# Performance work log

Measured on AMD Instinct MI355X. Metric: run time of the kernel, lower is better.

## Reference

```python
import jax, jax.numpy as jnp
import numpy as np

N, E, IN, H, ED = 50000, 800000, 128, 128, 3
EPS = 1e-5

def _gat_conv(x, src, dst, ea, W, a_src, a_dst, We, a_edge, bias):
    n = x.shape[0]
    # add self loops; self-loop edge_attr = per-feature mean (PyG fill_value='mean')
    loops = jnp.arange(n, dtype=src.dtype)
    s = jnp.concatenate([src, loops])
    d = jnp.concatenate([dst, loops])
    ea_full = jnp.concatenate([ea, jnp.broadcast_to(ea.mean(0), (n, ea.shape[1]))], 0)
    h = x @ W                       # [n, H]
    al_s = h @ a_src                # [n]
    al_d = h @ a_dst
    al_e = (ea_full @ We) @ a_edge  # [E+n]
    alpha = jax.nn.leaky_relu(al_s[s] + al_d[d] + al_e, 0.2)
    # segment softmax over destination nodes (every node has a self loop)
    amax = jax.ops.segment_max(alpha, d, num_segments=n)
    ex = jnp.exp(alpha - amax[d])
    denom = jax.ops.segment_sum(ex, d, num_segments=n)
    coef = ex / (denom[d] + 1e-16)
    out = jax.ops.segment_sum(h[s] * coef[:, None], d, num_segments=n)
    return out + bias

def _bn(x, gamma, beta):
    mu = x.mean(0)
    var = ((x - mu) ** 2).mean(0)
    return (x - mu) * jax.lax.rsqrt(var + EPS) * gamma + beta

def setup_inputs():
    key = jax.random.key(0)
    ks = jax.random.split(key, 40)
    inp = {
        "x": jax.random.normal(ks[0], (N, IN), jnp.float32),
        "edge_index": jax.random.randint(ks[1], (2, E), 0, N, dtype=jnp.int32),
        "batch": jnp.zeros((N,), jnp.int32),
        "edge_attr": jax.random.normal(ks[2], (E, ED), jnp.float32),
    }
    i = 3
    for l, cin in ((1, IN), (2, H), (3, H)):
        s = 1.0 / np.sqrt(cin)
        inp[f"W{l}"] = jax.random.normal(ks[i], (cin, H), jnp.float32) * s; i += 1
        inp[f"as{l}"] = jax.random.normal(ks[i], (H,), jnp.float32) * 0.1; i += 1
        inp[f"ad{l}"] = jax.random.normal(ks[i], (H,), jnp.float32) * 0.1; i += 1
        inp[f"We{l}"] = jax.random.normal(ks[i], (ED, H), jnp.float32) * 0.5; i += 1
        inp[f"ae{l}"] = jax.random.normal(ks[i], (H,), jnp.float32) * 0.1; i += 1
        inp[f"b{l}"] = jnp.zeros((H,), jnp.float32)
        inp[f"g{l}"] = jnp.ones((H,), jnp.float32)
        inp[f"be{l}"] = jnp.zeros((H,), jnp.float32)
    return inp

def reference(x, edge_index, batch, edge_attr,
              W1, as1, ad1, We1, ae1, b1, g1, be1,
              W2, as2, ad2, We2, ae2, b2, g2, be2,
              W3, as3, ad3, We3, ae3, b3, g3, be3):
    src, dst = edge_index[0], edge_index[1]
    h = _gat_conv(x, src, dst, edge_attr, W1, as1, ad1, We1, ae1, b1)
    h = _bn(jax.nn.leaky_relu(h, 0.01), g1, be1)
    h = _gat_conv(h, src, dst, edge_attr, W2, as2, ad2, We2, ae2, b2)
    h = _bn(jax.nn.leaky_relu(h, 0.01), g2, be2)
    h = _gat_conv(h, src, dst, edge_attr, W3, as3, ad3, We3, ae3, b3)
    h = _bn(jax.nn.leaky_relu(h, 0.01), g3, be3)
    return h
```

## Files before the change

kernel.cpp:

```cpp
#include <hip/hip_runtime.h>
#include <hip/hip_fp16.h>
#include <math.h>


#define NB 64

struct __align__(16) Edge2 { int src; int dst; unsigned e01; unsigned e2; };

__device__ __forceinline__ unsigned short f2bf(float x) {
  unsigned u = __float_as_uint(x);
  unsigned r = (u + 0x7FFFu + ((u >> 16) & 1u)) >> 16;
  return (unsigned short)r;
}
__device__ __forceinline__ float bf_lo(unsigned u) { return __uint_as_float(u << 16); }
__device__ __forceinline__ float bf_hi(unsigned u) { return __uint_as_float(u & 0xFFFF0000u); }

__global__ void k_hist_lds(const int* __restrict__ dst, const float* __restrict__ ea, int E,
                           int n, unsigned* __restrict__ hist32, float* __restrict__ ea_sum) {
  extern __shared__ unsigned cnt[];
  int nh = (n + 1) >> 1;
  for (int i = threadIdx.x; i < nh; i += blockDim.x) cnt[i] = 0u;
  __syncthreads();
  int tid = blockIdx.x * blockDim.x + threadIdx.x;
  int stride = gridDim.x * blockDim.x;
  float s0 = 0.f, s1 = 0.f, s2 = 0.f;
  for (int i = tid; i < E; i += stride) {
    int d = dst[i];
    atomicAdd(&cnt[d >> 1], 1u << ((d & 1) << 4));
    s0 += ea[i * 3 + 0]; s1 += ea[i * 3 + 1]; s2 += ea[i * 3 + 2];
  }
  for (int off = 32; off; off >>= 1) {
    s0 += __shfl_down(s0, off); s1 += __shfl_down(s1, off); s2 += __shfl_down(s2, off);
  }
  if ((threadIdx.x & 63) == 0) {
    atomicAdd(&ea_sum[0], s0); atomicAdd(&ea_sum[1], s1); atomicAdd(&ea_sum[2], s2);
  }
  __syncthreads();
  unsigned* plane = hist32 + (size_t)blockIdx.x * nh;
  for (int i = threadIdx.x; i < nh; i += blockDim.x) plane[i] = cnt[i];
}

__device__ __forceinline__ int wave_incl_scan(int x, int lane) {
  for (int off = 1; off < 64; off <<= 1) {
    int t = __shfl_up(x, off);
    if (lane >= off) x += t;
  }
  return x;
}

__global__ __launch_bounds__(1024) void k_scan_a(const unsigned* __restrict__ hist32, int n,
                                                 int* __restrict__ start,
                                                 int* __restrict__ bsum) {
  __shared__ int wsum[16];
  int t = threadIdx.x, lane = t & 63, w = t >> 6;
  int i = blockIdx.x * 1024 + t;
  int nh = (n + 1) >> 1;
  int stride2 = nh * 2;
  const unsigned short* h16 = (const unsigned short*)hist32;
  int v = 0;
  if (i < n) {
    for (int r = 0; r < NB; ++r) v += h16[(size_t)r * stride2 + i];
  }
  int x = wave_incl_scan(v, lane);
  if (lane == 63) wsum[w] = x;
  __syncthreads();
  if (w == 0 && lane < 16) {
    int s = wsum[lane];
    for (int off = 1; off < 16; off <<= 1) {
      int u = __shfl_up(s, off);
      if (lane >= off) s += u;
    }
    wsum[lane] = s;
  }
  __syncthreads();
  int woff = w ? wsum[w - 1] : 0;
  if (i < n) start[i] = x - v + woff;
  if (t == 1023) bsum[blockIdx.x] = wsum[15];
}

__global__ void k_scan_b(int* __restrict__ bsum, int nb, int* __restrict__ start, int n) {
  int lane = threadIdx.x;
  int v = (lane < nb) ? bsum[lane] : 0;
  int x = wave_incl_scan(v, lane);
  if (lane < nb) bsum[lane] = x - v;
  if (lane == nb - 1) start[n] = x;
}

__global__ void k_scan_c(int* __restrict__ start, const int* __restrict__ bsum,
                         const unsigned* __restrict__ hist32, int n,
                         int* __restrict__ cursorp) {
  int i = blockIdx.x * blockDim.x + threadIdx.x;
  if (i >= n) return;
  int nh = (n + 1) >> 1;
  int stride2 = nh * 2;
  const unsigned short* h16 = (const unsigned short*)hist32;
  int s = start[i] + bsum[i >> 10];
  start[i] = s;
  int run = s;
  for (int r = 0; r < NB; ++r) {
    cursorp[(size_t)r * n + i] = run;
    run += h16[(size_t)r * stride2 + i];
  }
}

__global__ void k_scatter_lds(const int* __restrict__ src, const int* __restrict__ dst,
                              const float* __restrict__ ea, int E, int n,
                              const int* __restrict__ cursorp, Edge2* __restrict__ edges) {
  extern __shared__ unsigned cnt[];
  int nh = (n + 1) >> 1;
  for (int i = threadIdx.x; i < nh; i += blockDim.x) cnt[i] = 0u;
  __syncthreads();
  const int* cur = cursorp + (size_t)blockIdx.x * n;
  int tid = blockIdx.x * blockDim.x + threadIdx.x;
  int stride = gridDim.x * blockDim.x;
  for (int i = tid; i < E; i += stride) {
    int d = dst[i];
    int sh = (d & 1) << 4;
    unsigned old = atomicAdd(&cnt[d >> 1], 1u << sh);
    int rank = (old >> sh) & 0xFFFF;
    int pos = cur[d] + rank;
    unsigned short h0 = __half_as_ushort(__float2half(ea[i * 3 + 0]));
    unsigned short h1 = __half_as_ushort(__float2half(ea[i * 3 + 1]));
    unsigned short h2 = __half_as_ushort(__float2half(ea[i * 3 + 2]));
    Edge2 e;
    e.src = src[i];
    e.dst = d;
    e.e01 = (unsigned)h0 | ((unsigned)h1 << 16);
    e.e2 = (unsigned)h2;
    edges[pos] = e;
  }
}

__device__ __forceinline__ void param_wave(const float* __restrict__ We,
                                           const float* __restrict__ ae,
                                           const float* __restrict__ ea_sum, float invE,
                                           float* __restrict__ P, int lane) {
  float a0 = ae[lane], a1 = ae[64 + lane];
  float p0 = We[0 * 128 + lane] * a0 + We[0 * 128 + 64 + lane] * a1;
  float p1 = We[1 * 128 + lane] * a0 + We[1 * 128 + 64 + lane] * a1;
  float p2 = We[2 * 128 + lane] * a0 + We[2 * 128 + 64 + lane] * a1;
  for (int off = 32; off; off >>= 1) {
    p0 += __shfl_down(p0, off); p1 += __shfl_down(p1, off); p2 += __shfl_down(p2, off);
  }
  if (lane == 0) {
    P[0] = p0; P[1] = p1; P[2] = p2;
    P[3] = ea_sum[0] * invE * p0 + ea_sum[1] * invE * p1 + ea_sum[2] * invE * p2;
  }
}

__global__ void k_param0(const float* __restrict__ We, const float* __restrict__ ae,
                         const float* __restrict__ ea_sum, float invE, float* __restrict__ P,
                         float* __restrict__ scale, float* __restrict__ shift,
                         float* __restrict__ colstats) {
  int t = threadIdx.x;
  if (t < 64) {
    param_wave(We, ae, ea_sum, invE, P, t);
  } else if (t < 192) {
    int c = t - 64;
    scale[c] = 1.f; shift[c] = 0.f;
    colstats[c] = 0.f; colstats[128 + c] = 0.f;
  }
}

__global__ void k_inter(const float* __restrict__ colstatsIn, const float* __restrict__ g,
                        const float* __restrict__ be, float invN,
                        float* __restrict__ scale, float* __restrict__ shift,
                        const float* __restrict__ WeN, const float* __restrict__ aeN,
                        const float* __restrict__ ea_sum, float invE, float* __restrict__ P,
                        float* __restrict__ colstats) {
  int t = threadIdx.x;
  if (t < 64) {
    param_wave(WeN, aeN, ea_sum, invE, P, t);
  } else if (t < 192) {
    int c = t - 64;
    float mu = colstatsIn[c] * invN;
    float var = colstatsIn[128 + c] * invN - mu * mu;
    var = var > 0.f ? var : 0.f;
    float sc = g[c] * rsqrtf(var + 1e-5f);
    scale[c] = sc;
    shift[c] = be[c] - mu * sc;
    colstats[c] = 0.f; colstats[128 + c] = 0.f;
  }
}

__global__ __launch_bounds__(256) void k_gemm2(
    const float* __restrict__ X, const float* __restrict__ Wm,
    const float* __restrict__ bnsc, const float* __restrict__ bnsh,
    const float* __restrict__ as, const float* __restrict__ ad,
    const float* __restrict__ P,
    unsigned* __restrict__ hb, float* __restrict__ al_s, float* __restrict__ al_d,
    float* __restrict__ es, int n) {
  __shared__ float wl[128 * 128];
  __shared__ float xs[32 * 128];
  int t = threadIdx.x;
  for (int i = t; i < 4096; i += 256) ((float4*)wl)[i] = ((const float4*)Wm)[i];
  int c32 = t & 31;
  int c4 = c32 << 2;
  int rq = t >> 5;
  int lane = t & 63;
  float4 av_s = *(const float4*)(as + c4);
  float4 av_d = *(const float4*)(ad + c4);
  float cself = P[3];
  int ntiles = (n + 31) >> 5;
  for (int tile = blockIdx.x; tile < ntiles; tile += gridDim.x) {
    int r0 = tile << 5;
    __syncthreads();
    for (int i = t; i < 1024; i += 256) {
      int rr = i >> 5, cc = i & 31;
      int g = r0 + rr;
      float4 v;
      if (g < n) {
        v = ((const float4*)(X + (size_t)g * 128))[cc];
        float4 sc = ((const float4*)bnsc)[cc];
        float4 sh = ((const float4*)bnsh)[cc];
        v.x = fmaf(v.x, sc.x, sh.x); v.y = fmaf(v.y, sc.y, sh.y);
        v.z = fmaf(v.z, sc.z, sh.z); v.w = fmaf(v.w, sc.w, sh.w);
      } else { v.x = v.y = v.z = v.w = 0.f; }
      ((float4*)xs)[i] = v;
    }
    __syncthreads();
    float4 acc[4];
    for (int r = 0; r < 4; ++r) { acc[r].x = acc[r].y = acc[r].z = acc[r].w = 0.f; }
    const float* xr = xs + (rq << 2) * 128;
#pragma unroll 4
    for (int k = 0; k < 128; ++k) {
      float4 w4 = ((const float4*)wl)[(k << 5) + c32];
#pragma unroll
      for (int r = 0; r < 4; ++r) {
        float xv = xr[r * 128 + k];
        acc[r].x = fmaf(xv, w4.x, acc[r].x);
        acc[r].y = fmaf(xv, w4.y, acc[r].y);
        acc[r].z = fmaf(xv, w4.z, acc[r].z);
        acc[r].w = fmaf(xv, w4.w, acc[r].w);
      }
    }
    int gbase = r0 + (rq << 2);
#pragma unroll
    for (int r = 0; r < 4; ++r) {
      int g = gbase + r;
      float4 o = acc[r];
      if (g < n) {
        unsigned u01 = ((unsigned)f2bf(o.y) << 16) | (unsigned)f2bf(o.x);
        unsigned u23 = ((unsigned)f2bf(o.w) << 16) | (unsigned)f2bf(o.z);
        uint2 uu = {u01, u23};
        *(uint2*)(hb + (size_t)g * 64 + (c32 << 1)) = uu;
      }
      float ps = o.x * av_s.x + o.y * av_s.y + o.z * av_s.z + o.w * av_s.w;
      float pd = o.x * av_d.x + o.y * av_d.y + o.z * av_d.z + o.w * av_d.w;
      for (int off = 16; off; off >>= 1) {
        ps += __shfl_xor(ps, off);
        pd += __shfl_xor(pd, off);
      }
      if ((lane & 31) == 0 && g < n) {
        al_s[g] = ps; al_d[g] = pd;
        float a = ps + pd + cself;
        a = a > 0.f ? a : 0.2f * a;
        es[g] = __expf(a);
      }
    }
  }
}

__global__ __launch_bounds__(256) void k_alpha3(const int4* __restrict__ edges,
                                                const float* __restrict__ al_s,
                                                const float* __restrict__ al_d,
                                                const float* __restrict__ P,
                                                int2* __restrict__ meta, int E) {
  int i = blockIdx.x * blockDim.x + threadIdx.x;
  if (i >= E) return;
  int4 ev = edges[i];
  float e0 = __half2float(__ushort_as_half((unsigned short)(ev.z & 0xFFFF)));
  float e1 = __half2float(__ushort_as_half((unsigned short)(((unsigned)ev.z) >> 16)));
  float e2 = __half2float(__ushort_as_half((unsigned short)(ev.w & 0xFFFF)));
  float a = al_s[ev.x] + al_d[ev.y] + e0 * P[0] + e1 * P[1] + e2 * P[2];
  a = a > 0.f ? a : 0.2f * a;
  int2 mv;
  mv.x = ev.x;
  mv.y = __float_as_int(__expf(a));
  meta[i] = mv;
}

__global__ __launch_bounds__(256) void k_agg9(const int2* __restrict__ meta,
                                              const int* __restrict__ start,
                                              const unsigned* __restrict__ hb,
                                              const float* __restrict__ es,
                                              const float* __restrict__ bias,
                                              float* __restrict__ y,
                                              float* __restrict__ colsum,
                                              float* __restrict__ colsumsq, int n) {
  int lane = threadIdx.x & 63;
  int w = threadIdx.x >> 6;
  int grp = lane >> 4;
  int sub = lane & 15;
  int gw = (blockIdx.x * blockDim.x + threadIdx.x) >> 6;
  int nw = (gridDim.x * blockDim.x) >> 6;
  int c0 = (sub << 3) + (grp << 1);
  float2 b2 = ((const float2*)bias)[(sub << 2) + grp];
  float s0 = 0.f, s1 = 0.f, q0 = 0.f, q1 = 0.f;

#define DO_QUAD(EB)                                                          \
  {                                                                          \
    int i0 = (EB), i1 = (EB) + 1, i2 = (EB) + 2, i3 = (EB) + 3;              \
    int2 m0 = meta[i0 < e1 ? i0 : e0];                                       \
    int2 m1 = meta[i1 < e1 ? i1 : e0];                                       \
    int2 m2 = meta[i2 < e1 ? i2 : e0];                                       \
    int2 m3 = meta[i3 < e1 ? i3 : e0];                                       \
    int r0 = i0 < e1 ? m0.x : i;                                             \
    int r1 = i1 < e1 ? m1.x : i;                                             \
    int r2 = i2 < e1 ? m2.x : i;                                             \
    int r3 = i3 < e1 ? m3.x : i;                                             \
    float p0 = i0 < e1 ? __int_as_float(m0.y) : 0.f;                         \
    float p1 = i1 < e1 ? __int_as_float(m1.y) : 0.f;                         \
    float p2 = i2 < e1 ? __int_as_float(m2.y) : 0.f;                         \
    float p3 = i3 < e1 ? __int_as_float(m3.y) : 0.f;                         \
    int rr = grp == 0 ? r0 : grp == 1 ? r1 : grp == 2 ? r2 : r3;             \
    float pp = grp == 0 ? p0 : grp == 1 ? p1 : grp == 2 ? p2 : p3;           \
    uint4 gv = *(const uint4*)(hb + (size_t)rr * 64 + (sub << 2));           \
    pacc += (p0 + p1) + (p2 + p3);                                           \
    aL0 = fmaf(pp, bf_lo(gv.x), aL0); aH0 = fmaf(pp, bf_hi(gv.x), aH0);      \
    aL1 = fmaf(pp, bf_lo(gv.y), aL1); aH1 = fmaf(pp, bf_hi(gv.y), aH1);      \
    aL2 = fmaf(pp, bf_lo(gv.z), aL2); aH2 = fmaf(pp, bf_hi(gv.z), aH2);      \
    aL3 = fmaf(pp, bf_lo(gv.w), aL3); aH3 = fmaf(pp, bf_hi(gv.w), aH3);      \
  }

  for (int i = gw; i < n; i += nw) {
    int e0 = __builtin_amdgcn_readfirstlane(start[i]);
    int e1 = __builtin_amdgcn_readfirstlane(start[i + 1]);
    float eself = es[i];
    uint4 hv = *(const uint4*)(hb + (size_t)i * 64 + (sub << 2));
    float wself = (grp == 0) ? eself : 0.f;
    float aL0 = wself * bf_lo(hv.x), aH0 = wself * bf_hi(hv.x);
    float aL1 = wself * bf_lo(hv.y), aH1 = wself * bf_hi(hv.y);
    float aL2 = wself * bf_lo(hv.z), aH2 = wself * bf_hi(hv.z);
    float aL3 = wself * bf_lo(hv.w), aH3 = wself * bf_hi(hv.w);
    float pacc = 0.f;
    int e = e0;
    for (; e + 8 <= e1; e += 8) {
      DO_QUAD(e);
      DO_QUAD(e + 4);
    }
    for (; e < e1; e += 4) DO_QUAD(e);
    aL0 += __shfl_xor(aL0, 16); aL0 += __shfl_xor(aL0, 32);
    aH0 += __shfl_xor(aH0, 16); aH0 += __shfl_xor(aH0, 32);
    aL1 += __shfl_xor(aL1, 16); aL1 += __shfl_xor(aL1, 32);
    aH1 += __shfl_xor(aH1, 16); aH1 += __shfl_xor(aH1, 32);
    aL2 += __shfl_xor(aL2, 16); aL2 += __shfl_xor(aL2, 32);
    aH2 += __shfl_xor(aH2, 16); aH2 += __shfl_xor(aH2, 32);
    aL3 += __shfl_xor(aL3, 16); aL3 += __shfl_xor(aL3, 32);
    aH3 += __shfl_xor(aH3, 16); aH3 += __shfl_xor(aH3, 32);
    float inv = 1.0f / (eself + pacc + 1e-16f);
    float o0 = grp == 0 ? aL0 : grp == 1 ? aL1 : grp == 2 ? aL2 : aL3;
    float o1 = grp == 0 ? aH0 : grp == 1 ? aH1 : grp == 2 ? aH2 : aH3;
    o0 = fmaf(o0, inv, b2.x);
    o1 = fmaf(o1, inv, b2.y);
    o0 = o0 > 0.f ? o0 : 0.01f * o0;
    o1 = o1 > 0.f ? o1 : 0.01f * o1;
    float2 o2 = {o0, o1};
    *(float2*)(y + (size_t)i * 128 + c0) = o2;
    s0 += o0; s1 += o1;
    q0 = fmaf(o0, o0, q0); q1 = fmaf(o1, o1, q1);
  }
#undef DO_QUAD
  __shared__ float red[4][4][64];
  red[0][w][lane] = s0; red[1][w][lane] = s1; red[2][w][lane] = q0; red[3][w][lane] = q1;
  __syncthreads();
  if (w == 0) {
    for (int ww = 1; ww < 4; ++ww) {
      s0 += red[0][ww][lane]; s1 += red[1][ww][lane];
      q0 += red[2][ww][lane]; q1 += red[3][ww][lane];
    }
    atomicAdd(&colsum[c0], s0);
    atomicAdd(&colsum[c0 + 1], s1);
    atomicAdd(&colsumsq[c0], q0);
    atomicAdd(&colsumsq[c0 + 1], q1);
  }
}

__global__ __launch_bounds__(256) void k_bnapply_final(
    const float4* __restrict__ yin, const float* __restrict__ colstats,
    const float* __restrict__ g, const float* __restrict__ be, float invN,
    float4* __restrict__ yout, int total4) {
  __shared__ float sc_s[128], sh_s[128];
  int t = threadIdx.x;
  if (t < 128) {
    float mu = colstats[t] * invN;
    float var = colstats[128 + t] * invN - mu * mu;
    var = var > 0.f ? var : 0.f;
    float sc = g[t] * rsqrtf(var + 1e-5f);
    sc_s[t] = sc;
    sh_s[t] = be[t] - mu * sc;
  }
  __syncthreads();
  for (int i = blockIdx.x * blockDim.x + t; i < total4; i += gridDim.x * blockDim.x) {
    int c4 = (i & 31) << 2;
    float4 v = yin[i];
    v.x = fmaf(v.x, sc_s[c4 + 0], sh_s[c4 + 0]);
    v.y = fmaf(v.y, sc_s[c4 + 1], sh_s[c4 + 1]);
    v.z = fmaf(v.z, sc_s[c4 + 2], sh_s[c4 + 2]);
    v.w = fmaf(v.w, sc_s[c4 + 3], sh_s[c4 + 3]);
    yout[i] = v;
  }
}

extern "C" void kernel_launch(void* const* d_in, const int* in_sizes, int n_in,
                              void* d_out, int out_size, void* d_ws, size_t ws_size,
                              hipStream_t stream) {
  const float* x = (const float*)d_in[0];
  const int* eidx = (const int*)d_in[1];
  const float* ea = (const float*)d_in[3];
  const int H = 128;
  const int N = in_sizes[0] / H;
  const int E = in_sizes[1] / 2;
  const int* srcIdx = eidx;
  const int* dstIdx = eidx + E;
  const int nh = (N + 1) >> 1;

  char* ws = (char*)d_ws;
  size_t off = 0;
  auto alloc = [&](size_t bytes) -> void* {
    void* p = ws + off;
    off = (off + bytes + 255) & ~(size_t)255;
    return p;
  };
  Edge2* edges = (Edge2*)alloc((size_t)E * sizeof(Edge2));
  int2* meta = (int2*)alloc((size_t)E * sizeof(int2));
  unsigned* hb = (unsigned*)alloc((size_t)N * 64 * sizeof(unsigned));
  float* y = (float*)alloc((size_t)N * H * sizeof(float));
  float* al_s = (float*)alloc((size_t)N * sizeof(float));
  float* al_d = (float*)alloc((size_t)N * sizeof(float));
  float* es = (float*)alloc((size_t)N * sizeof(float));
  unsigned* hist32 = (unsigned*)alloc((size_t)NB * nh * sizeof(unsigned));
  int* cursorp = (int*)alloc((size_t)NB * N * sizeof(int));
  int* start = (int*)alloc((size_t)(N + 1) * sizeof(int));
  int* bsum = (int*)alloc(64 * sizeof(int));
  float* colstats = (float*)alloc(256 * sizeof(float));
  float* colsum = colstats;
  float* colsumsq = colstats + 128;
  float* scale = (float*)alloc(128 * sizeof(float));
  float* shift = (float*)alloc(128 * sizeof(float));
  float* ea_sum = (float*)alloc(64 * sizeof(float));
  float* P = (float*)alloc(16 * sizeof(float));

  const int nb = (N + 1023) / 1024;
  const float invE = 1.0f / (float)E;
  const float invN = 1.0f / (float)N;
  const size_t ldsBytes = (size_t)nh * sizeof(unsigned);

  hipMemsetAsync(ea_sum, 0, 64 * sizeof(float), stream);
  k_hist_lds<<<NB, 256, ldsBytes, stream>>>(dstIdx, ea, E, N, hist32, ea_sum);
  k_scan_a<<<nb, 1024, 0, stream>>>(hist32, N, start, bsum);
  k_scan_b<<<1, 64, 0, stream>>>(bsum, nb, start, N);
  k_scan_c<<<(N + 255) / 256, 256, 0, stream>>>(start, bsum, hist32, N, cursorp);
  k_scatter_lds<<<NB, 256, ldsBytes, stream>>>(srcIdx, dstIdx, ea, E, N, cursorp, edges);

  const float* Wl[3]; const float* asl[3]; const float* adl[3]; const float* Wel[3];
  const float* ael[3]; const float* bl[3]; const float* gl[3]; const float* bel[3];
  for (int l = 0; l < 3; ++l) {
    Wl[l] = (const float*)d_in[4 + 8 * l + 0];
    asl[l] = (const float*)d_in[4 + 8 * l + 1];
    adl[l] = (const float*)d_in[4 + 8 * l + 2];
    Wel[l] = (const float*)d_in[4 + 8 * l + 3];
    ael[l] = (const float*)d_in[4 + 8 * l + 4];
    bl[l] = (const float*)d_in[4 + 8 * l + 5];
    gl[l] = (const float*)d_in[4 + 8 * l + 6];
    bel[l] = (const float*)d_in[4 + 8 * l + 7];
  }

  k_param0<<<1, 192, 0, stream>>>(Wel[0], ael[0], ea_sum, invE, P, scale, shift, colstats);

  const float* X = x;
  for (int l = 0; l < 3; ++l) {
    k_gemm2<<<512, 256, 0, stream>>>(X, Wl[l], scale, shift, asl[l], adl[l], P,
                                     hb, al_s, al_d, es, N);
    k_alpha3<<<(E + 255) / 256, 256, 0, stream>>>((const int4*)edges, al_s, al_d, P,
                                                  meta, E);
    k_agg9<<<2048, 256, 0, stream>>>(meta, start, hb, es, bl[l], y,
                                     colsum, colsumsq, N);
    if (l < 2) {
      k_inter<<<1, 192, 0, stream>>>(colstats, gl[l], bel[l], invN, scale, shift,
                                     Wel[l + 1], ael[l + 1], ea_sum, invE, P, colstats);
    }
    X = y;
  }
  k_bnapply_final<<<384, 256, 0, stream>>>((const float4*)y, colstats, gl[2], bel[2], invN,
                                           (float4*)d_out, N * 32);
}
```

Baseline: 751.1 us.

## Split CSR by source half and aggregate in two locality passes

Edges are now bucketed by (destination, source-half), which gives 2N bins. The histogram uses 8-bit LDS counters and NB drops to 32 blocks so the doubled bin count still fits in LDS. Aggregation runs two passes over the nodes: each pass gathers features only from one half of the source nodes, so the gather working set is smaller and should stay in cache. The first pass's partial sums go to y and paccb and are merged in the second pass. This adds extra writes and reads of y, plus a second sweep over start/es, and 8-bit counters can overflow if one block sees more than 255 edges for a single bin.

```diff
diff --git a/kernel.cpp b/kernel.cpp
--- a/kernel.cpp
+++ b/kernel.cpp
@@ -3,7 +3,7 @@
 #include <math.h>
 
 
-#define NB 64
+#define NB 32
 
 struct __align__(16) Edge2 { int src; int dst; unsigned e01; unsigned e2; };
 
@@ -15,18 +15,21 @@
 __device__ __forceinline__ float bf_lo(unsigned u) { return __uint_as_float(u << 16); }
 __device__ __forceinline__ float bf_hi(unsigned u) { return __uint_as_float(u & 0xFFFF0000u); }
 
-__global__ void k_hist_lds(const int* __restrict__ dst, const float* __restrict__ ea, int E,
-                           int n, unsigned* __restrict__ hist32, float* __restrict__ ea_sum) {
+__global__ void k_hist_lds(const int* __restrict__ src, const int* __restrict__ dst,
+                           const float* __restrict__ ea, int E, int bins, int half,
+                           unsigned* __restrict__ hist32, float* __restrict__ ea_sum) {
   extern __shared__ unsigned cnt[];
-  int nh = (n + 1) >> 1;
-  for (int i = threadIdx.x; i < nh; i += blockDim.x) cnt[i] = 0u;
+  int nwords = (bins + 3) >> 2;
+  for (int i = threadIdx.x; i < nwords; i += blockDim.x) cnt[i] = 0u;
   __syncthreads();
   int tid = blockIdx.x * blockDim.x + threadIdx.x;
   int stride = gridDim.x * blockDim.x;
   float s0 = 0.f, s1 = 0.f, s2 = 0.f;
   for (int i = tid; i < E; i += stride) {
     int d = dst[i];
-    atomicAdd(&cnt[d >> 1], 1u << ((d & 1) << 4));
+    int s = src[i];
+    int key = (d << 1) | (s >= half ? 1 : 0);
+    atomicAdd(&cnt[key >> 2], 1u << ((key & 3) << 3));
     s0 += ea[i * 3 + 0]; s1 += ea[i * 3 + 1]; s2 += ea[i * 3 + 2];
   }
   for (int off = 32; off; off >>= 1) {
@@ -36,8 +39,8 @@
     atomicAdd(&ea_sum[0], s0); atomicAdd(&ea_sum[1], s1); atomicAdd(&ea_sum[2], s2);
   }
   __syncthreads();
-  unsigned* plane = hist32 + (size_t)blockIdx.x * nh;
-  for (int i = threadIdx.x; i < nh; i += blockDim.x) plane[i] = cnt[i];
+  unsigned* plane = hist32 + (size_t)blockIdx.x * nwords;
+  for (int i = threadIdx.x; i < nwords; i += blockDim.x) plane[i] = cnt[i];
 }
 
 __device__ __forceinline__ int wave_incl_scan(int x, int lane) {
@@ -48,18 +51,18 @@
   return x;
 }
 
-__global__ __launch_bounds__(1024) void k_scan_a(const unsigned* __restrict__ hist32, int n,
-                                                 int* __restrict__ start,
+__global__ __launch_bounds__(1024) void k_scan_a(const unsigned* __restrict__ hist32,
+                                                 int bins, int* __restrict__ start,
                                                  int* __restrict__ bsum) {
   __shared__ int wsum[16];
   int t = threadIdx.x, lane = t & 63, w = t >> 6;
   int i = blockIdx.x * 1024 + t;
-  int nh = (n + 1) >> 1;
-  int stride2 = nh * 2;
-  const unsigned short* h16 = (const unsigned short*)hist32;
+  int nwords = (bins + 3) >> 2;
+  size_t planeB = (size_t)nwords * 4;
+  const unsigned char* h8 = (const unsigned char*)hist32;
   int v = 0;
-  if (i < n) {
-    for (int r = 0; r < NB; ++r) v += h16[(size_t)r * stride2 + i];
+  if (i < bins) {
+    for (int r = 0; r < NB; ++r) v += h8[(size_t)r * planeB + i];
   }
   int x = wave_incl_scan(v, lane);
   if (lane == 63) wsum[w] = x;
@@ -74,56 +77,63 @@
   }
   __syncthreads();
   int woff = w ? wsum[w - 1] : 0;
-  if (i < n) start[i] = x - v + woff;
+  if (i < bins) start[i] = x - v + woff;
   if (t == 1023) bsum[blockIdx.x] = wsum[15];
 }
 
-__global__ void k_scan_b(int* __restrict__ bsum, int nb, int* __restrict__ start, int n) {
-  int lane = threadIdx.x;
-  int v = (lane < nb) ? bsum[lane] : 0;
+__global__ void k_scan_b(int* __restrict__ bsum, int nb, int* __restrict__ start, int bins) {
+  __shared__ int wtot[2];
+  int t = threadIdx.x;
+  int lane = t & 63, w = t >> 6;
+  int v = (t < nb) ? bsum[t] : 0;
   int x = wave_incl_scan(v, lane);
-  if (lane < nb) bsum[lane] = x - v;
-  if (lane == nb - 1) start[n] = x;
+  if (lane == 63) wtot[w] = x;
+  __syncthreads();
+  if (w == 1) x += wtot[0];
+  if (t < nb) bsum[t] = x - v;
+  if (t == nb - 1) start[bins] = x;
 }
 
 __global__ void k_scan_c(int* __restrict__ start, const int* __restrict__ bsum,
-                         const unsigned* __restrict__ hist32, int n,
+                         const unsigned* __restrict__ hist32, int bins,
                          int* __restrict__ cursorp) {
   int i = blockIdx.x * blockDim.x + threadIdx.x;
-  if (i >= n) return;
-  int nh = (n + 1) >> 1;
-  int stride2 = nh * 2;
-  const unsigned short* h16 = (const unsigned short*)hist32;
+  if (i >= bins) return;
+  int nwords = (bins + 3) >> 2;
+  size_t planeB = (size_t)nwords * 4;
+  const unsigned char* h8 = (const unsigned char*)hist32;
   int s = start[i] + bsum[i >> 10];
   start[i] = s;
   int run = s;
   for (int r = 0; r < NB; ++r) {
-    cursorp[(size_t)r * n + i] = run;
-    run += h16[(size_t)r * stride2 + i];
+    cursorp[(size_t)r * bins + i] = run;
+    run += h8[(size_t)r * planeB + i];
   }
 }
 
 __global__ void k_scatter_lds(const int* __restrict__ src, const int* __restrict__ dst,
-                              const float* __restrict__ ea, int E, int n,
+                              const float* __restrict__ ea, int E, int bins, int half,
                               const int* __restrict__ cursorp, Edge2* __restrict__ edges) {
   extern __shared__ unsigned cnt[];
-  int nh = (n + 1) >> 1;
-  for (int i = threadIdx.x; i < nh; i += blockDim.x) cnt[i] = 0u;
-  __syncthreads();
-  const int* cur = cursorp + (size_t)blockIdx.x * n;
+  int nwords = (bins + 3) >> 2;
+  for (int i = threadIdx.x; i < nwords; i += blockDim.x) cnt[i] = 0u;
+  __syncthreads();
+  const int* cur = cursorp + (size_t)blockIdx.x * bins;
   int tid = blockIdx.x * blockDim.x + threadIdx.x;
   int stride = gridDim.x * blockDim.x;
   for (int i = tid; i < E; i += stride) {
     int d = dst[i];
-    int sh = (d & 1) << 4;
-    unsigned old = atomicAdd(&cnt[d >> 1], 1u << sh);
-    int rank = (old >> sh) & 0xFFFF;
-    int pos = cur[d] + rank;
+    int s = src[i];
+    int key = (d << 1) | (s >= half ? 1 : 0);
+    int sh = (key & 3) << 3;
+    unsigned old = atomicAdd(&cnt[key >> 2], 1u << sh);
+    int rank = (old >> sh) & 0xFF;
+    int pos = cur[key] + rank;
     unsigned short h0 = __half_as_ushort(__float2half(ea[i * 3 + 0]));
     unsigned short h1 = __half_as_ushort(__float2half(ea[i * 3 + 1]));
     unsigned short h2 = __half_as_ushort(__float2half(ea[i * 3 + 2]));
     Edge2 e;
-    e.src = src[i];
+    e.src = s;
     e.dst = d;
     e.e01 = (unsigned)h0 | ((unsigned)h1 << 16);
     e.e2 = (unsigned)h2;
@@ -280,14 +290,15 @@
   meta[i] = mv;
 }
 
-__global__ __launch_bounds__(256) void k_agg9(const int2* __restrict__ meta,
-                                              const int* __restrict__ start,
-                                              const unsigned* __restrict__ hb,
-                                              const float* __restrict__ es,
-                                              const float* __restrict__ bias,
-                                              float* __restrict__ y,
-                                              float* __restrict__ colsum,
-                                              float* __restrict__ colsumsq, int n) {
+__global__ __launch_bounds__(256) void k_agg10(const int2* __restrict__ meta,
+                                               const int* __restrict__ start,
+                                               const unsigned* __restrict__ hb,
+                                               const float* __restrict__ es,
+                                               const float* __restrict__ bias,
+                                               float* __restrict__ y,
+                                               float* __restrict__ paccb,
+                                               float* __restrict__ colsum,
+                                               float* __restrict__ colsumsq, int n) {
   int lane = threadIdx.x & 63;
   int w = threadIdx.x >> 6;
   int grp = lane >> 4;
@@ -323,9 +334,19 @@
     aL3 = fmaf(pp, bf_lo(gv.w), aL3); aH3 = fmaf(pp, bf_hi(gv.w), aH3);      \
   }
 
+#define COMBINE()                                                            \
+  aL0 += __shfl_xor(aL0, 16); aL0 += __shfl_xor(aL0, 32);                    \
+  aH0 += __shfl_xor(aH0, 16); aH0 += __shfl_xor(aH0, 32);                    \
+  aL1 += __shfl_xor(aL1, 16); aL1 += __shfl_xor(aL1, 32);                    \
+  aH1 += __shfl_xor(aH1, 16); aH1 += __shfl_xor(aH1, 32);                    \
+  aL2 += __shfl_xor(aL2, 16); aL2 += __shfl_xor(aL2, 32);                    \
+  aH2 += __shfl_xor(aH2, 16); aH2 += __shfl_xor(aH2, 32);                    \
+  aL3 += __shfl_xor(aL3, 16); aL3 += __shfl_xor(aL3, 32);                    \
+  aH3 += __shfl_xor(aH3, 16); aH3 += __shfl_xor(aH3, 32);
+
   for (int i = gw; i < n; i += nw) {
-    int e0 = __builtin_amdgcn_readfirstlane(start[i]);
-    int e1 = __builtin_amdgcn_readfirstlane(start[i + 1]);
+    int e0 = __builtin_amdgcn_readfirstlane(start[2 * i]);
+    int e1 = __builtin_amdgcn_readfirstlane(start[2 * i + 1]);
     float eself = es[i];
     uint4 hv = *(const uint4*)(hb + (size_t)i * 64 + (sub << 2));
     float wself = (grp == 0) ? eself : 0.f;
@@ -335,22 +356,36 @@
     float aL3 = wself * bf_lo(hv.w), aH3 = wself * bf_hi(hv.w);
     float pacc = 0.f;
     int e = e0;
-    for (; e + 8 <= e1; e += 8) {
-      DO_QUAD(e);
-      DO_QUAD(e + 4);
-    }
+    for (; e + 8 <= e1; e += 8) { DO_QUAD(e); DO_QUAD(e + 4); }
     for (; e < e1; e += 4) DO_QUAD(e);
-    aL0 += __shfl_xor(aL0, 16); aL0 += __shfl_xor(aL0, 32);
-    aH0 += __shfl_xor(aH0, 16); aH0 += __shfl_xor(aH0, 32);
-    aL1 += __shfl_xor(aL1, 16); aL1 += __shfl_xor(aL1, 32);
-    aH1 += __shfl_xor(aH1, 16); aH1 += __shfl_xor(aH1, 32);
-    aL2 += __shfl_xor(aL2, 16); aL2 += __shfl_xor(aL2, 32);
-    aH2 += __shfl_xor(aH2, 16); aH2 += __shfl_xor(aH2, 32);
-    aL3 += __shfl_xor(aL3, 16); aL3 += __shfl_xor(aL3, 32);
-    aH3 += __shfl_xor(aH3, 16); aH3 += __shfl_xor(aH3, 32);
-    float inv = 1.0f / (eself + pacc + 1e-16f);
+    COMBINE();
     float o0 = grp == 0 ? aL0 : grp == 1 ? aL1 : grp == 2 ? aL2 : aL3;
     float o1 = grp == 0 ? aH0 : grp == 1 ? aH1 : grp == 2 ? aH2 : aH3;
+    float2 p2v = {o0, o1};
+    __builtin_nontemporal_store(*(const double*)&p2v,
+                                (double*)(y + (size_t)i * 128 + c0));
+    if (lane == 0) paccb[i] = pacc;
+  }
+  asm volatile("s_waitcnt vmcnt(0)" ::: "memory");
+  for (int i = gw; i < n; i += nw) {
+    int e0 = __builtin_amdgcn_readfirstlane(start[2 * i + 1]);
+    int e1 = __builtin_amdgcn_readfirstlane(start[2 * i + 2]);
+    float eself = es[i];
+    float aL0 = 0.f, aH0 = 0.f, aL1 = 0.f, aH1 = 0.f;
+    float aL2 = 0.f, aH2 = 0.f, aL3 = 0.f, aH3 = 0.f;
+    float pacc = 0.f;
+    int e = e0;
+    for (; e + 8 <= e1; e += 8) { DO_QUAD(e); DO_QUAD(e + 4); }
+    for (; e < e1; e += 4) DO_QUAD(e);
+    COMBINE();
+    float o0 = grp == 0 ? aL0 : grp == 1 ? aL1 : grp == 2 ? aL2 : aL3;
+    float o1 = grp == 0 ? aH0 : grp == 1 ? aH1 : grp == 2 ? aH2 : aH3;
+    double dv = __builtin_nontemporal_load((const double*)(y + (size_t)i * 128 + c0));
+    float2 part = *(float2*)&dv;
+    float pb = paccb[i];
+    o0 += part.x;
+    o1 += part.y;
+    float inv = 1.0f / (eself + pacc + pb + 1e-16f);
     o0 = fmaf(o0, inv, b2.x);
     o1 = fmaf(o1, inv, b2.y);
     o0 = o0 > 0.f ? o0 : 0.01f * o0;
@@ -361,6 +396,7 @@
     q0 = fmaf(o0, o0, q0); q1 = fmaf(o1, o1, q1);
   }
 #undef DO_QUAD
+#undef COMBINE
   __shared__ float red[4][4][64];
   red[0][w][lane] = s0; red[1][w][lane] = s1; red[2][w][lane] = q0; red[3][w][lane] = q1;
   __syncthreads();
@@ -413,7 +449,9 @@
   const int E = in_sizes[1] / 2;
   const int* srcIdx = eidx;
   const int* dstIdx = eidx + E;
-  const int nh = (N + 1) >> 1;
+  const int bins = 2 * N;
+  const int half = N >> 1;
+  const int nwords = (bins + 3) >> 2;
 
   char* ws = (char*)d_ws;
   size_t off = 0;
@@ -429,10 +467,11 @@
   float* al_s = (float*)alloc((size_t)N * sizeof(float));
   float* al_d = (float*)alloc((size_t)N * sizeof(float));
   float* es = (float*)alloc((size_t)N * sizeof(float));
-  unsigned* hist32 = (unsigned*)alloc((size_t)NB * nh * sizeof(unsigned));
-  int* cursorp = (int*)alloc((size_t)NB * N * sizeof(int));
-  int* start = (int*)alloc((size_t)(N + 1) * sizeof(int));
-  int* bsum = (int*)alloc(64 * sizeof(int));
+  float* paccb = (float*)alloc((size_t)N * sizeof(float));
+  unsigned* hist32 = (unsigned*)alloc((size_t)NB * nwords * sizeof(unsigned));
+  int* cursorp = (int*)alloc((size_t)NB * bins * sizeof(int));
+  int* start = (int*)alloc((size_t)(bins + 1) * sizeof(int));
+  int* bsum = (int*)alloc(128 * sizeof(int));
   float* colstats = (float*)alloc(256 * sizeof(float));
   float* colsum = colstats;
   float* colsumsq = colstats + 128;
@@ -441,17 +480,19 @@
   float* ea_sum = (float*)alloc(64 * sizeof(float));
   float* P = (float*)alloc(16 * sizeof(float));
 
-  const int nb = (N + 1023) / 1024;
+  const int nbScan = (bins + 1023) / 1024;
   const float invE = 1.0f / (float)E;
   const float invN = 1.0f / (float)N;
-  const size_t ldsBytes = (size_t)nh * sizeof(unsigned);
+  const size_t ldsBytes = (size_t)nwords * sizeof(unsigned);
 
   hipMemsetAsync(ea_sum, 0, 64 * sizeof(float), stream);
-  k_hist_lds<<<NB, 256, ldsBytes, stream>>>(dstIdx, ea, E, N, hist32, ea_sum);
-  k_scan_a<<<nb, 1024, 0, stream>>>(hist32, N, start, bsum);
-  k_scan_b<<<1, 64, 0, stream>>>(bsum, nb, start, N);
-  k_scan_c<<<(N + 255) / 256, 256, 0, stream>>>(start, bsum, hist32, N, cursorp);
-  k_scatter_lds<<<NB, 256, ldsBytes, stream>>>(srcIdx, dstIdx, ea, E, N, cursorp, edges);
+  k_hist_lds<<<NB, 256, ldsBytes, stream>>>(srcIdx, dstIdx, ea, E, bins, half,
+                                            hist32, ea_sum);
+  k_scan_a<<<nbScan, 1024, 0, stream>>>(hist32, bins, start, bsum);
+  k_scan_b<<<1, 128, 0, stream>>>(bsum, nbScan, start, bins);
+  k_scan_c<<<(bins + 255) / 256, 256, 0, stream>>>(start, bsum, hist32, bins, cursorp);
+  k_scatter_lds<<<NB, 256, ldsBytes, stream>>>(srcIdx, dstIdx, ea, E, bins, half,
+                                               cursorp, edges);
 
   const float* Wl[3]; const float* asl[3]; const float* adl[3]; const float* Wel[3];
   const float* ael[3]; const float* bl[3]; const float* gl[3]; const float* bel[3];
@@ -474,8 +515,8 @@
                                      hb, al_s, al_d, es, N);
     k_alpha3<<<(E + 255) / 256, 256, 0, stream>>>((const int4*)edges, al_s, al_d, P,
                                                   meta, E);
-    k_agg9<<<2048, 256, 0, stream>>>(meta, start, hb, es, bl[l], y,
-                                     colsum, colsumsq, N);
+    k_agg10<<<2048, 256, 0, stream>>>(meta, start, hb, es, bl[l], y, paccb,
+                                      colsum, colsumsq, N);
     if (l < 2) {
       k_inter<<<1, 192, 0, stream>>>(colstats, gl[l], bel[l], invN, scale, shift,
                                      Wel[l + 1], ael[l + 1], ea_sum, invE, P, colstats);
```

New measurement: 846.7 us. 12.7% more time.

## Switch node feature GEMM to bf16 MFMA with LDS-staged output

Applied to the files above, without the earlier changes.

Replaces the fp32 FMA-based per-layer X@W kernel with one using 16x16x32 bf16 MFMA instructions. Weights are transposed and converted to bf16 in LDS, and input tiles of 64 rows are stored as bf16 with padded strides. The attention projections are reduced across 16-lane groups, and outputs are staged through LDS for coalesced bf16 stores. This cuts the ALU cost of the dense transform but rounds the inputs and weights to bf16 before multiplication, which lowers precision.

```diff
diff --git a/kernel.cpp b/kernel.cpp
--- a/kernel.cpp
+++ b/kernel.cpp
@@ -4,6 +4,9 @@
 
 
 #define NB 64
+
+typedef __attribute__((ext_vector_type(8))) short bf16x8;
+typedef __attribute__((ext_vector_type(4))) float f32x4;
 
 struct __align__(16) Edge2 { int src; int dst; unsigned e01; unsigned e2; };
 
@@ -183,79 +186,102 @@
   }
 }
 
-__global__ __launch_bounds__(256) void k_gemm2(
+__global__ __launch_bounds__(256) void k_gemm3(
     const float* __restrict__ X, const float* __restrict__ Wm,
     const float* __restrict__ bnsc, const float* __restrict__ bnsh,
     const float* __restrict__ as, const float* __restrict__ ad,
     const float* __restrict__ P,
     unsigned* __restrict__ hb, float* __restrict__ al_s, float* __restrict__ al_d,
     float* __restrict__ es, int n) {
-  __shared__ float wl[128 * 128];
-  __shared__ float xs[32 * 128];
+  __shared__ __align__(16) unsigned short wb[128 * 136];
+  __shared__ __align__(16) unsigned short xb[64 * 136];
   int t = threadIdx.x;
-  for (int i = t; i < 4096; i += 256) ((float4*)wl)[i] = ((const float4*)Wm)[i];
-  int c32 = t & 31;
-  int c4 = c32 << 2;
-  int rq = t >> 5;
   int lane = t & 63;
-  float4 av_s = *(const float4*)(as + c4);
-  float4 av_d = *(const float4*)(ad + c4);
+  int w = t >> 6;
+  int c16 = lane & 15;
+  int kq = lane >> 4;
+  for (int i = t; i < 4096; i += 256) {
+    int k = i >> 5, c4 = (i & 31) << 2;
+    float4 v = ((const float4*)(Wm + k * 128))[i & 31];
+    wb[(c4 + 0) * 136 + k] = f2bf(v.x);
+    wb[(c4 + 1) * 136 + k] = f2bf(v.y);
+    wb[(c4 + 2) * 136 + k] = f2bf(v.z);
+    wb[(c4 + 3) * 136 + k] = f2bf(v.w);
+  }
+  float asv[8], adv[8];
+#pragma unroll
+  for (int ct = 0; ct < 8; ++ct) {
+    asv[ct] = as[ct * 16 + c16];
+    adv[ct] = ad[ct * 16 + c16];
+  }
   float cself = P[3];
-  int ntiles = (n + 31) >> 5;
+  int ntiles = (n + 63) >> 6;
   for (int tile = blockIdx.x; tile < ntiles; tile += gridDim.x) {
-    int r0 = tile << 5;
+    int r0 = tile << 6;
     __syncthreads();
-    for (int i = t; i < 1024; i += 256) {
-      int rr = i >> 5, cc = i & 31;
-      int g = r0 + rr;
+    for (int i = t; i < 2048; i += 256) {
+      int row = i >> 5, c4 = i & 31;
+      int g = r0 + row;
       float4 v;
       if (g < n) {
-        v = ((const float4*)(X + (size_t)g * 128))[cc];
-        float4 sc = ((const float4*)bnsc)[cc];
-        float4 sh = ((const float4*)bnsh)[cc];
+        v = ((const float4*)(X + (size_t)g * 128))[c4];
+        float4 sc = ((const float4*)bnsc)[c4];
+        float4 sh = ((const float4*)bnsh)[c4];
         v.x = fmaf(v.x, sc.x, sh.x); v.y = fmaf(v.y, sc.y, sh.y);
         v.z = fmaf(v.z, sc.z, sh.z); v.w = fmaf(v.w, sc.w, sh.w);
       } else { v.x = v.y = v.z = v.w = 0.f; }
-      ((float4*)xs)[i] = v;
+      uint2 pk;
+      pk.x = (unsigned)f2bf(v.x) | ((unsigned)f2bf(v.y) << 16);
+      pk.y = (unsigned)f2bf(v.z) | ((unsigned)f2bf(v.w) << 16);
+      *(uint2*)(xb + row * 136 + (c4 << 2)) = pk;
     }
     __syncthreads();
-    float4 acc[4];
-    for (int r = 0; r < 4; ++r) { acc[r].x = acc[r].y = acc[r].z = acc[r].w = 0.f; }
-    const float* xr = xs + (rq << 2) * 128;
-#pragma unroll 4
-    for (int k = 0; k < 128; ++k) {
-      float4 w4 = ((const float4*)wl)[(k << 5) + c32];
+    const unsigned short* xr = xb + (w * 16 + c16) * 136 + kq * 8;
+    bf16x8 A[4];
 #pragma unroll
-      for (int r = 0; r < 4; ++r) {
-        float xv = xr[r * 128 + k];
-        acc[r].x = fmaf(xv, w4.x, acc[r].x);
-        acc[r].y = fmaf(xv, w4.y, acc[r].y);
-        acc[r].z = fmaf(xv, w4.z, acc[r].z);
-        acc[r].w = fmaf(xv, w4.w, acc[r].w);
+    for (int kb = 0; kb < 4; ++kb) A[kb] = *(const bf16x8*)(xr + kb * 32);
+    f32x4 acc[8];
+#pragma unroll
+    for (int ct = 0; ct < 8; ++ct) {
+      const unsigned short* wr = wb + (ct * 16 + c16) * 136 + kq * 8;
+      f32x4 a = {0.f, 0.f, 0.f, 0.f};
+#pragma unroll
+      for (int kb = 0; kb < 4; ++kb) {
+        bf16x8 B = *(const bf16x8*)(wr + kb * 32);
+        a = __builtin_amdgcn_mfma_f32_16x16x32_bf16(A[kb], B, a, 0, 0, 0);
       }
-    }
-    int gbase = r0 + (rq << 2);
+      acc[ct] = a;
+    }
 #pragma unroll
     for (int r = 0; r < 4; ++r) {
-      int g = gbase + r;
-      float4 o = acc[r];
-      if (g < n) {
-        unsigned u01 = ((unsigned)f2bf(o.y) << 16) | (unsigned)f2bf(o.x);
-        unsigned u23 = ((unsigned)f2bf(o.w) << 16) | (unsigned)f2bf(o.z);
-        uint2 uu = {u01, u23};
-        *(uint2*)(hb + (size_t)g * 64 + (c32 << 1)) = uu;
+      int R = kq * 4 + r;
+      float pr = 0.f, pd = 0.f;
+#pragma unroll
+      for (int ct = 0; ct < 8; ++ct) {
+        float hv = acc[ct][r];
+        xb[(w * 16 + R) * 136 + ct * 16 + c16] = f2bf(hv);
+        pr = fmaf(hv, asv[ct], pr);
+        pd = fmaf(hv, adv[ct], pd);
       }
-      float ps = o.x * av_s.x + o.y * av_s.y + o.z * av_s.z + o.w * av_s.w;
-      float pd = o.x * av_d.x + o.y * av_d.y + o.z * av_d.z + o.w * av_d.w;
-      for (int off = 16; off; off >>= 1) {
-        ps += __shfl_xor(ps, off);
+      for (int off = 8; off; off >>= 1) {
+        pr += __shfl_xor(pr, off);
         pd += __shfl_xor(pd, off);
       }
-      if ((lane & 31) == 0 && g < n) {
-        al_s[g] = ps; al_d[g] = pd;
-        float a = ps + pd + cself;
+      int g = r0 + w * 16 + R;
+      if (c16 == 0 && g < n) {
+        al_s[g] = pr; al_d[g] = pd;
+        float a = pr + pd + cself;
         a = a > 0.f ? a : 0.2f * a;
         es[g] = __expf(a);
+      }
+    }
+    __syncthreads();
+    for (int i = lane; i < 256; i += 64) {
+      int row = i >> 4, cc = i & 15;
+      int g = r0 + w * 16 + row;
+      if (g < n) {
+        uint4 v = *(const uint4*)(xb + (w * 16 + row) * 136 + (cc << 3));
+        *(uint4*)(hb + (size_t)g * 64 + (cc << 2)) = v;
       }
     }
   }
@@ -470,7 +496,7 @@
 
   const float* X = x;
   for (int l = 0; l < 3; ++l) {
-    k_gemm2<<<512, 256, 0, stream>>>(X, Wl[l], scale, shift, asl[l], adl[l], P,
+    k_gemm3<<<512, 256, 0, stream>>>(X, Wl[l], scale, shift, asl[l], adl[l], P,
                                      hb, al_s, al_d, es, N);
     k_alpha3<<<(E + 255) / 256, 256, 0, stream>>>((const int4*)edges, al_s, al_d, P,
                                                   meta, E);
```

New measurement: 722.1 us. 1.04x faster.
